# Kernel tuning notes

Measured on AMD Instinct MI355X. Metric: run time of the kernel, lower is better.

The kernel has to match this reference:

```python
import jax, jax.numpy as jnp
import numpy as np

B, T, H, V = 4, 1024, 2048, 32000
BETA, EPS_LO, EPS_HI, TEMP = 0.1, 0.2, 0.2, 1.0


def setup_inputs() -> dict:
    key = jax.random.key(0)
    ks = jax.random.split(key, 7)
    x = jax.random.normal(ks[0], (B, T, H), jnp.float32)
    ref_input = jax.random.normal(ks[1], (B, T, H), jnp.float32)
    lin_weight = jax.random.normal(ks[2], (V, H), jnp.float32) * 0.02
    ref_lin_weight = jax.random.normal(ks[3], (V, H), jnp.float32) * 0.02
    selected_token_ids = jax.random.randint(ks[4], (B, T), 0, V, dtype=jnp.int32)
    attention_mask = jnp.ones((B, T), jnp.int32)
    advantages = jax.random.normal(ks[5], (B,), jnp.float32)
    # plausible stale log-probs near -log(V) so importance ratio ~ 1
    old_per_token_logps = jax.random.normal(ks[6], (B, T), jnp.float32) * 0.05 - float(np.log(V))
    return dict(x=x, ref_input=ref_input, lin_weight=lin_weight,
                ref_lin_weight=ref_lin_weight, selected_token_ids=selected_token_ids,
                attention_mask=attention_mask, advantages=advantages,
                old_per_token_logps=old_per_token_logps)


def _per_token_logps(h, W, ids):
    # fused linear + log-softmax, gathered at the sampled token ids
    logits = jnp.einsum('bth,vh->btv', h, W) / TEMP          # (B,T,V)
    lse = jax.nn.logsumexp(logits, axis=-1)                   # (B,T)
    sel = jnp.take_along_axis(logits, ids[..., None], axis=-1)[..., 0]
    return sel - lse


def reference(x, ref_input, lin_weight, ref_lin_weight, selected_token_ids,
              attention_mask, advantages, old_per_token_logps):
    per_token_logps = _per_token_logps(x, lin_weight, selected_token_ids)
    # reference model runs without grad in the original (torch.no_grad)
    ref_logps = jax.lax.stop_gradient(
        _per_token_logps(ref_input, ref_lin_weight, selected_token_ids))

    coef1 = jnp.exp(per_token_logps - old_per_token_logps)   # importance ratio
    coef2 = jnp.clip(coef1, 1.0 - EPS_LO, 1.0 + EPS_HI)
    adv = advantages[:, None]                                 # (B,1)
    per_token_loss = -jnp.minimum(coef1 * adv, coef2 * adv)

    delta = ref_logps - per_token_logps
    kl = jnp.exp(delta) - delta - 1.0                         # k3 KL estimator
    per_token_loss = per_token_loss + BETA * kl

    m = attention_mask.astype(per_token_loss.dtype)
    loss = jnp.sum(per_token_loss * m) / jnp.maximum(jnp.sum(m), 1.0)
    return loss
```

## Files before the change

kernel.cpp:

```cpp
#include <hip/hip_runtime.h>
#include <hip/hip_bf16.h>
#include <stdint.h>

#define B_    4
#define T_    1024
#define H_    2048
#define V_    32000
#define M_TOK (B_ * T_)
#define BM    128
#define BN    128
#define BK    32
#define NVT   (V_ / BN)
#define KITER (H_ / BK)
#define BETA_   0.1f
#define EPS_LO_ 0.2f
#define EPS_HI_ 0.2f

typedef __bf16 bf16x8 __attribute__((ext_vector_type(8)));
typedef float  f32x4  __attribute__((ext_vector_type(4)));

__device__ __forceinline__ void load16_lds(const void* g, void* l) {
    __builtin_amdgcn_global_load_lds(
        (const __attribute__((address_space(1))) unsigned int*)g,
        (__attribute__((address_space(3))) unsigned int*)l, 16, 0, 0);
}

__device__ __forceinline__ unsigned short f2bf(float f) {
    unsigned u = __float_as_uint(f);
    u += 0x7FFF + ((u >> 16) & 1);
    return (unsigned short)(u >> 16);
}
__device__ __forceinline__ unsigned pack2(float a, float b) {
    return (unsigned)f2bf(a) | ((unsigned)f2bf(b) << 16);
}

__global__ __launch_bounds__(256) void cvt_bf16(const float4* __restrict__ in,
                                                uint4* __restrict__ out, int n8) {
    int i = blockIdx.x * blockDim.x + threadIdx.x;
    if (i >= n8) return;
    float4 a = in[2 * i];
    float4 b = in[2 * i + 1];
    uint4 r;
    r.x = pack2(a.x, a.y);
    r.y = pack2(a.z, a.w);
    r.z = pack2(b.x, b.y);
    r.w = pack2(b.z, b.w);
    out[i] = r;
}

__global__ __launch_bounds__(256, 2) void gemm_lse(
    const unsigned short* __restrict__ Xp, const unsigned short* __restrict__ Wp,
    const unsigned short* __restrict__ Xr, const unsigned short* __restrict__ Wr,
    const int* __restrict__ ids,
    float* __restrict__ part_p, float* __restrict__ part_r,
    float* __restrict__ sel_p,  float* __restrict__ sel_r)
{
    const int tid  = threadIdx.x;
    const int lane = tid & 63;
    const int wid  = tid >> 6;
    const int wm   = wid >> 1;
    const int wn   = wid & 1;
    const int tm   = blockIdx.x;
    const int tn   = blockIdx.y;
    const int z    = blockIdx.z;

    const unsigned short* X = z ? Xr : Xp;
    const unsigned short* W = z ? Wr : Wp;
    float* part = z ? part_r : part_p;
    float* sel  = z ? sel_r  : sel_p;

    const int rowA = tm * BM;
    const int colB = tn * BN;

    __shared__ __align__(16) unsigned short As[BM * BK];
    __shared__ __align__(16) unsigned short Bs[BN * BK];
    __shared__ float sums_s[2][BM];
    __shared__ int   ids_s[BM];

    if (tid < BM) ids_s[tid] = ids[rowA + tid];

    const int lrow = lane >> 2;
    const int lk   = (lane & 3) * 8;
    const unsigned short* gA0 = X + (size_t)(rowA + (wid)     * 16 + lrow) * H_ + lk;
    const unsigned short* gA1 = X + (size_t)(rowA + (4 + wid) * 16 + lrow) * H_ + lk;
    const unsigned short* gB0 = W + (size_t)(colB + (wid)     * 16 + lrow) * H_ + lk;
    const unsigned short* gB1 = W + (size_t)(colB + (4 + wid) * 16 + lrow) * H_ + lk;
    unsigned short* lA0 = &As[(wid)     * 16 * BK];
    unsigned short* lA1 = &As[(4 + wid) * 16 * BK];
    unsigned short* lB0 = &Bs[(wid)     * 16 * BK];
    unsigned short* lB1 = &Bs[(4 + wid) * 16 * BK];

    const int fr_row = lane & 15;
    const int fr_k   = (lane >> 4) * 8;

    f32x4 acc[4][4] = {};

    for (int kt = 0; kt < KITER; ++kt) {
        __syncthreads();
        load16_lds(gA0, lA0);
        load16_lds(gA1, lA1);
        load16_lds(gB0, lB0);
        load16_lds(gB1, lB1);
        gA0 += BK; gA1 += BK; gB0 += BK; gB1 += BK;
        __syncthreads();

        bf16x8 av[4], bv[4];
        #pragma unroll
        for (int f = 0; f < 4; ++f) {
            av[f] = *(const bf16x8*)&As[(wm * 64 + f * 16 + fr_row) * BK + fr_k];
            bv[f] = *(const bf16x8*)&Bs[(wn * 64 + f * 16 + fr_row) * BK + fr_k];
        }
        #pragma unroll
        for (int fm = 0; fm < 4; ++fm)
            #pragma unroll
            for (int fn = 0; fn < 4; ++fn)
                acc[fm][fn] = __builtin_amdgcn_mfma_f32_16x16x32_bf16(
                    av[fm], bv[fn], acc[fm][fn], 0, 0, 0);
    }

    const int lq = lane >> 4;
    const int ln = lane & 15;
    float rs[4][4];
    #pragma unroll
    for (int fm = 0; fm < 4; ++fm) {
        #pragma unroll
        for (int reg = 0; reg < 4; ++reg) {
            const int row_l = wm * 64 + fm * 16 + lq * 4 + reg;
            const int id    = ids_s[row_l];
            float s = 0.f;
            #pragma unroll
            for (int fn = 0; fn < 4; ++fn) {
                float v = acc[fm][fn][reg];
                int col_g = colB + wn * 64 + fn * 16 + ln;
                if (id == col_g) sel[rowA + row_l] = v;
                s += __expf(v);
            }
            rs[fm][reg] = s;
        }
    }
    #pragma unroll
    for (int m = 1; m < 16; m <<= 1) {
        #pragma unroll
        for (int fm = 0; fm < 4; ++fm)
            #pragma unroll
            for (int reg = 0; reg < 4; ++reg)
                rs[fm][reg] += __shfl_xor(rs[fm][reg], m, 64);
    }
    if (ln == 0) {
        #pragma unroll
        for (int fm = 0; fm < 4; ++fm)
            #pragma unroll
            for (int reg = 0; reg < 4; ++reg)
                sums_s[wn][wm * 64 + fm * 16 + lq * 4 + reg] = rs[fm][reg];
    }
    __syncthreads();
    if (tid < BM) {
        float tot = sums_s[0][tid] + sums_s[1][tid];
        part[(size_t)(rowA + tid) * NVT + tn] = tot;
    }
}

__global__ __launch_bounds__(256) void finalize(
    const float* __restrict__ pp, const float* __restrict__ pr,
    const float* __restrict__ sp, const float* __restrict__ sr,
    const int* __restrict__ mask, const float* __restrict__ adv,
    const float* __restrict__ oldlp,
    float* __restrict__ bsum, float* __restrict__ bmsum)
{
    const int lane = threadIdx.x & 63;
    const int wid  = threadIdx.x >> 6;
    const int t    = blockIdx.x * 4 + wid;

    float s_p = 0.f, s_r = 0.f;
    for (int i = lane; i < NVT; i += 64) {
        s_p += pp[(size_t)t * NVT + i];
        s_r += pr[(size_t)t * NVT + i];
    }
    #pragma unroll
    for (int k = 1; k < 64; k <<= 1) {
        s_p += __shfl_xor(s_p, k, 64);
        s_r += __shfl_xor(s_r, k, 64);
    }
    __shared__ float ls[4], ms[4];
    if (lane == 0) {
        float p  = sp[t] - logf(s_p);
        float r  = sr[t] - logf(s_r);
        float c1 = expf(p - oldlp[t]);
        float c2 = fminf(fmaxf(c1, 1.0f - EPS_LO_), 1.0f + EPS_HI_);
        float a  = adv[t >> 10];
        float ptl = -fminf(c1 * a, c2 * a);
        float d   = r - p;
        ptl += BETA_ * (expf(d) - d - 1.0f);
        float mm = (float)mask[t];
        ls[wid] = ptl * mm;
        ms[wid] = mm;
    }
    __syncthreads();
    if (threadIdx.x == 0) {
        bsum[blockIdx.x]  = ls[0] + ls[1] + ls[2] + ls[3];
        bmsum[blockIdx.x] = ms[0] + ms[1] + ms[2] + ms[3];
    }
}

__global__ __launch_bounds__(256) void final_reduce(
    const float* __restrict__ bs, const float* __restrict__ bm, float* __restrict__ out)
{
    const int tid = threadIdx.x;
    float s = 0.f, m = 0.f;
    for (int i = tid; i < M_TOK / 4; i += 256) { s += bs[i]; m += bm[i]; }
    #pragma unroll
    for (int k = 1; k < 64; k <<= 1) {
        s += __shfl_xor(s, k, 64);
        m += __shfl_xor(m, k, 64);
    }
    __shared__ float ss[4], sm[4];
    if ((tid & 63) == 0) { ss[tid >> 6] = s; sm[tid >> 6] = m; }
    __syncthreads();
    if (tid == 0) {
        float S = ss[0] + ss[1] + ss[2] + ss[3];
        float M = sm[0] + sm[1] + sm[2] + sm[3];
        out[0] = S / fmaxf(M, 1.0f);
    }
}

extern "C" void kernel_launch(void* const* d_in, const int* in_sizes, int n_in,
                              void* d_out, int out_size, void* d_ws, size_t ws_size,
                              hipStream_t stream) {
    const float* x     = (const float*)d_in[0];
    const float* rx    = (const float*)d_in[1];
    const float* w     = (const float*)d_in[2];
    const float* rw    = (const float*)d_in[3];
    const int*   ids   = (const int*)d_in[4];
    const int*   mask  = (const int*)d_in[5];
    const float* adv   = (const float*)d_in[6];
    const float* oldlp = (const float*)d_in[7];
    float* out = (float*)d_out;

    char* ws = (char*)d_ws;
    size_t off = 0;
    auto alloc = [&](size_t bytes) -> void* {
        void* p = ws + off;
        off += (bytes + 255) & ~(size_t)255;
        return p;
    };
    unsigned short* xb   = (unsigned short*)alloc((size_t)M_TOK * H_ * 2);
    unsigned short* rxb  = (unsigned short*)alloc((size_t)M_TOK * H_ * 2);
    unsigned short* wb   = (unsigned short*)alloc((size_t)V_ * H_ * 2);
    unsigned short* rwb  = (unsigned short*)alloc((size_t)V_ * H_ * 2);
    float* pp    = (float*)alloc((size_t)M_TOK * NVT * 4);
    float* pr    = (float*)alloc((size_t)M_TOK * NVT * 4);
    float* sp    = (float*)alloc((size_t)M_TOK * 4);
    float* sr    = (float*)alloc((size_t)M_TOK * 4);
    float* bsum  = (float*)alloc((M_TOK / 4) * 4);
    float* bmsum = (float*)alloc((M_TOK / 4) * 4);

    const int n8x = M_TOK * H_ / 8;
    const int n8w = V_ * H_ / 8;
    cvt_bf16<<<(n8x + 255) / 256, 256, 0, stream>>>((const float4*)x,  (uint4*)xb,  n8x);
    cvt_bf16<<<(n8x + 255) / 256, 256, 0, stream>>>((const float4*)rx, (uint4*)rxb, n8x);
    cvt_bf16<<<(n8w + 255) / 256, 256, 0, stream>>>((const float4*)w,  (uint4*)wb,  n8w);
    cvt_bf16<<<(n8w + 255) / 256, 256, 0, stream>>>((const float4*)rw, (uint4*)rwb, n8w);

    dim3 grid(M_TOK / BM, V_ / BN, 2);
    gemm_lse<<<grid, 256, 0, stream>>>(xb, wb, rxb, rwb, ids, pp, pr, sp, sr);

    finalize<<<M_TOK / 4, 256, 0, stream>>>(pp, pr, sp, sr, mask, adv, oldlp, bsum, bmsum);
    final_reduce<<<1, 256, 0, stream>>>(bsum, bmsum, out);
}
```

Measured before the change: 1.719 ms.

## Rebuild GEMM as 256x256x64 double-buffered, swizzled-LDS, 8-wave pipelined kernel

The fused GEMM+logsumexp kernel grows its tile from 128x128x32 with 4 waves to 256x256x64 with 8 waves. It double-buffers LDS with XOR-swizzled layouts and interleaves global-to-LDS staging with four MFMA phases per k-step, using s_setprio and explicit vmcnt waits. The aim is to raise arithmetic intensity per byte loaded, cut LDS bank conflicts, and hide memory latency behind MFMA work. In exchange it adds more barriers per iteration and much higher register and LDS pressure, and the hand-tuned pipeline is fragile. The epilogue reuses the staging LDS for ids and partial sums, and the last k-step clamps its prefetch index.

```diff
diff --git a/kernel.cpp b/kernel.cpp
--- a/kernel.cpp
+++ b/kernel.cpp
@@ -7,11 +7,13 @@
 #define H_    2048
 #define V_    32000
 #define M_TOK (B_ * T_)
-#define BM    128
-#define BN    128
-#define BK    32
+#define BM    256
+#define BN    256
+#define BK    64
 #define NVT   (V_ / BN)
-#define KITER (H_ / BK)
+#define KT    (H_ / BK)
+#define KT2   (KT / 2)
+#define TILE_E (BM * BK)
 #define BETA_   0.1f
 #define EPS_LO_ 0.2f
 #define EPS_HI_ 0.2f
@@ -48,7 +50,7 @@
     out[i] = r;
 }
 
-__global__ __launch_bounds__(256, 2) void gemm_lse(
+__global__ __launch_bounds__(512, 2) void gemm_lse(
     const unsigned short* __restrict__ Xp, const unsigned short* __restrict__ Wp,
     const unsigned short* __restrict__ Xr, const unsigned short* __restrict__ Wr,
     const int* __restrict__ ids,
@@ -58,8 +60,8 @@
     const int tid  = threadIdx.x;
     const int lane = tid & 63;
     const int wid  = tid >> 6;
-    const int wm   = wid >> 1;
-    const int wn   = wid & 1;
+    const int wm   = wid >> 2;
+    const int wn   = wid & 3;
     const int tm   = blockIdx.x;
     const int tn   = blockIdx.y;
     const int z    = blockIdx.z;
@@ -72,90 +74,177 @@
     const int rowA = tm * BM;
     const int colB = tn * BN;
 
-    __shared__ __align__(16) unsigned short As[BM * BK];
-    __shared__ __align__(16) unsigned short Bs[BN * BK];
-    __shared__ float sums_s[2][BM];
-    __shared__ int   ids_s[BM];
-
-    if (tid < BM) ids_s[tid] = ids[rowA + tid];
-
-    const int lrow = lane >> 2;
-    const int lk   = (lane & 3) * 8;
-    const unsigned short* gA0 = X + (size_t)(rowA + (wid)     * 16 + lrow) * H_ + lk;
-    const unsigned short* gA1 = X + (size_t)(rowA + (4 + wid) * 16 + lrow) * H_ + lk;
-    const unsigned short* gB0 = W + (size_t)(colB + (wid)     * 16 + lrow) * H_ + lk;
-    const unsigned short* gB1 = W + (size_t)(colB + (4 + wid) * 16 + lrow) * H_ + lk;
-    unsigned short* lA0 = &As[(wid)     * 16 * BK];
-    unsigned short* lA1 = &As[(4 + wid) * 16 * BK];
-    unsigned short* lB0 = &Bs[(wid)     * 16 * BK];
-    unsigned short* lB1 = &Bs[(4 + wid) * 16 * BK];
-
-    const int fr_row = lane & 15;
-    const int fr_k   = (lane >> 4) * 8;
-
-    f32x4 acc[4][4] = {};
-
-    for (int kt = 0; kt < KITER; ++kt) {
-        __syncthreads();
-        load16_lds(gA0, lA0);
-        load16_lds(gA1, lA1);
-        load16_lds(gB0, lB0);
-        load16_lds(gB1, lB1);
-        gA0 += BK; gA1 += BK; gB0 += BK; gB1 += BK;
-        __syncthreads();
-
-        bf16x8 av[4], bv[4];
-        #pragma unroll
-        for (int f = 0; f < 4; ++f) {
-            av[f] = *(const bf16x8*)&As[(wm * 64 + f * 16 + fr_row) * BK + fr_k];
-            bv[f] = *(const bf16x8*)&Bs[(wn * 64 + f * 16 + fr_row) * BK + fr_k];
-        }
-        #pragma unroll
-        for (int fm = 0; fm < 4; ++fm)
-            #pragma unroll
-            for (int fn = 0; fn < 4; ++fn)
-                acc[fm][fn] = __builtin_amdgcn_mfma_f32_16x16x32_bf16(
-                    av[fm], bv[fn], acc[fm][fn], 0, 0, 0);
-    }
-
-    const int lq = lane >> 4;
-    const int ln = lane & 15;
-    float rs[4][4];
+    __shared__ __align__(16) unsigned short As[2 * TILE_E];
+    __shared__ __align__(16) unsigned short Bs[2 * TILE_E];
+
+    const int g0 = wid * 2;
+    const int lr = lane >> 3;
+    const int ls = lane & 7;
+    const int so = (ls ^ lr) * 8;
+    const int a0 = (g0 >> 3) * 128 + (g0 & 7) * 8;
+    const int b0 = (g0 >> 2) * 64  + (g0 & 3) * 8;
+    const unsigned short* pA[2];
+    const unsigned short* pB[2];
+    pA[0] = X + (size_t)(rowA + a0 + lr) * H_ + so;
+    pA[1] = pA[0] + (size_t)64 * H_;
+    pB[0] = W + (size_t)(colB + b0 + lr) * H_ + so;
+    pB[1] = pB[0] + (size_t)32 * H_;
+    const int aL[2] = { a0 * BK, a0 * BK + 64 * BK };
+    const int bL[2] = { b0 * BK, b0 * BK + 32 * BK };
+
+    const int lo = lane & 15;
+    const int hi = lane >> 4;
+    const int offs0 = ((hi) ^ (lane & 7)) * 8;
+    const int offs1 = offs0 ^ 32;
+
+    bf16x8 aR[4][2];
+    bf16x8 bR[2][2][2];
+    f32x4  acc[8][4] = {};
+
+#define FENCE() asm volatile("" ::: "memory")
+#define BARRIER() do { FENCE(); __builtin_amdgcn_s_barrier(); FENCE(); } while (0)
+
+#define STAGE_A(H, BUF, KOFF) do { \
+    load16_lds(pA[H] + (KOFF),          &As[(BUF)*TILE_E + aL[H]]); \
+    load16_lds(pA[H] + 8*H_ + (KOFF),   &As[(BUF)*TILE_E + aL[H] + 8*BK]); \
+} while (0)
+#define STAGE_B(H, BUF, KOFF) do { \
+    load16_lds(pB[H] + (KOFF),          &Bs[(BUF)*TILE_E + bL[H]]); \
+    load16_lds(pB[H] + 8*H_ + (KOFF),   &Bs[(BUF)*TILE_E + bL[H] + 8*BK]); \
+} while (0)
+
+#define RD_A(QM, BUF) do { \
+    _Pragma("unroll") \
+    for (int fmi = 0; fmi < 4; ++fmi) { \
+        const unsigned short* p_ = &As[(BUF)*TILE_E + (wm*128 + ((QM)*4 + fmi)*16 + lo)*BK]; \
+        aR[fmi][0] = *(const bf16x8*)(p_ + offs0); \
+        aR[fmi][1] = *(const bf16x8*)(p_ + offs1); \
+    } \
+} while (0)
+#define RD_B(QN, BUF) do { \
+    _Pragma("unroll") \
+    for (int fni = 0; fni < 2; ++fni) { \
+        const unsigned short* p_ = &Bs[(BUF)*TILE_E + (wn*64 + ((QN)*2 + fni)*16 + lo)*BK]; \
+        bR[QN][fni][0] = *(const bf16x8*)(p_ + offs0); \
+        bR[QN][fni][1] = *(const bf16x8*)(p_ + offs1); \
+    } \
+} while (0)
+
+#define MFMA16(QM, QN) do { \
+    _Pragma("unroll") \
+    for (int fmi = 0; fmi < 4; ++fmi) { \
+        _Pragma("unroll") \
+        for (int fni = 0; fni < 2; ++fni) { \
+            f32x4 c_ = acc[(QM)*4 + fmi][(QN)*2 + fni]; \
+            c_ = __builtin_amdgcn_mfma_f32_16x16x32_bf16(aR[fmi][0], bR[QN][fni][0], c_, 0, 0, 0); \
+            c_ = __builtin_amdgcn_mfma_f32_16x16x32_bf16(aR[fmi][1], bR[QN][fni][1], c_, 0, 0, 0); \
+            acc[(QM)*4 + fmi][(QN)*2 + fni] = c_; \
+        } \
+    } \
+} while (0)
+
+#define MFMA_PHASE(QM, QN) do { \
+    BARRIER(); \
+    __builtin_amdgcn_s_setprio(1); \
+    MFMA16(QM, QN); \
+    __builtin_amdgcn_s_setprio(0); \
+} while (0)
+
+    STAGE_A(0, 0, 0);
+    STAGE_B(0, 0, 0);
+    STAGE_B(1, 0, 0);
+    STAGE_A(1, 0, 0);
+    STAGE_A(0, 1, BK);
+    STAGE_B(0, 1, BK);
+    STAGE_B(1, 1, BK);
+    asm volatile("s_waitcnt vmcnt(6)" ::: "memory");
+    BARRIER();
+
+    for (int i = 0; i < KT2; ++i) {
+        const int k1 = (2 * i + 1) * BK;
+        const int k2 = (2 * i + 2 < KT ? 2 * i + 2 : KT - 1) * BK;
+        const int k3 = (2 * i + 3 < KT ? 2 * i + 3 : KT - 1) * BK;
+        RD_A(0, 0); RD_B(0, 0);
+        STAGE_A(1, 1, k1);
+        MFMA_PHASE(0, 0);
+        BARRIER();
+        RD_B(1, 0);
+        STAGE_A(0, 0, k2);
+        MFMA_PHASE(0, 1);
+        BARRIER();
+        RD_A(1, 0);
+        STAGE_B(0, 0, k2);
+        MFMA_PHASE(1, 0);
+        BARRIER();
+        STAGE_B(1, 0, k2);
+        MFMA_PHASE(1, 1);
+        asm volatile("s_waitcnt vmcnt(6)" ::: "memory");
+        BARRIER();
+        RD_A(0, 1); RD_B(0, 1);
+        STAGE_A(1, 0, k2);
+        MFMA_PHASE(0, 0);
+        BARRIER();
+        RD_B(1, 1);
+        STAGE_A(0, 1, k3);
+        MFMA_PHASE(0, 1);
+        BARRIER();
+        RD_A(1, 1);
+        STAGE_B(0, 1, k3);
+        MFMA_PHASE(1, 0);
+        BARRIER();
+        STAGE_B(1, 1, k3);
+        MFMA_PHASE(1, 1);
+        asm volatile("s_waitcnt vmcnt(6)" ::: "memory");
+        BARRIER();
+    }
+
+#undef FENCE
+#undef BARRIER
+#undef STAGE_A
+#undef STAGE_B
+#undef RD_A
+#undef RD_B
+#undef MFMA16
+#undef MFMA_PHASE
+
+    __syncthreads();
+    float* sums_f = (float*)As;
+    int*   ids_e  = (int*)Bs;
+    if (tid < BM) ids_e[tid] = ids[rowA + tid];
+    __syncthreads();
+
     #pragma unroll
-    for (int fm = 0; fm < 4; ++fm) {
+    for (int fm = 0; fm < 8; ++fm) {
+        float r4[4];
         #pragma unroll
         for (int reg = 0; reg < 4; ++reg) {
-            const int row_l = wm * 64 + fm * 16 + lq * 4 + reg;
-            const int id    = ids_s[row_l];
+            const int row_l = wm * 128 + fm * 16 + hi * 4 + reg;
+            const int id    = ids_e[row_l];
             float s = 0.f;
             #pragma unroll
             for (int fn = 0; fn < 4; ++fn) {
                 float v = acc[fm][fn][reg];
-                int col_g = colB + wn * 64 + fn * 16 + ln;
+                int col_g = colB + wn * 64 + fn * 16 + lo;
                 if (id == col_g) sel[rowA + row_l] = v;
                 s += __expf(v);
             }
-            rs[fm][reg] = s;
+            r4[reg] = s;
         }
-    }
-    #pragma unroll
-    for (int m = 1; m < 16; m <<= 1) {
         #pragma unroll
-        for (int fm = 0; fm < 4; ++fm)
+        for (int m = 1; m < 16; m <<= 1) {
             #pragma unroll
             for (int reg = 0; reg < 4; ++reg)
-                rs[fm][reg] += __shfl_xor(rs[fm][reg], m, 64);
-    }
-    if (ln == 0) {
-        #pragma unroll
-        for (int fm = 0; fm < 4; ++fm)
+                r4[reg] += __shfl_xor(r4[reg], m, 64);
+        }
+        if (lo == 0) {
             #pragma unroll
             for (int reg = 0; reg < 4; ++reg)
-                sums_s[wn][wm * 64 + fm * 16 + lq * 4 + reg] = rs[fm][reg];
+                sums_f[wn * BM + wm * 128 + fm * 16 + hi * 4 + reg] = r4[reg];
+        }
     }
     __syncthreads();
     if (tid < BM) {
-        float tot = sums_s[0][tid] + sums_s[1][tid];
+        float tot = sums_f[tid] + sums_f[BM + tid] + sums_f[2 * BM + tid] + sums_f[3 * BM + tid];
         part[(size_t)(rowA + tid) * NVT + tn] = tot;
     }
 }
@@ -261,8 +350,8 @@
     cvt_bf16<<<(n8w + 255) / 256, 256, 0, stream>>>((const float4*)w,  (uint4*)wb,  n8w);
     cvt_bf16<<<(n8w + 255) / 256, 256, 0, stream>>>((const float4*)rw, (uint4*)rwb, n8w);
 
-    dim3 grid(M_TOK / BM, V_ / BN, 2);
-    gemm_lse<<<grid, 256, 0, stream>>>(xb, wb, rxb, rwb, ids, pp, pr, sp, sr);
+    dim3 grid(M_TOK / BM, NVT, 2);
+    gemm_lse<<<grid, 512, 0, stream>>>(xb, wb, rxb, rwb, ids, pp, pr, sp, sr);
 
     finalize<<<M_TOK / 4, 256, 0, stream>>>(pp, pr, sp, sr, mask, adv, oldlp, bsum, bmsum);
     final_reduce<<<1, 256, 0, stream>>>(bsum, bmsum, out);
```

After: 1.800 ms. 1.05x slower.
